# Performance work log

Measured on AMD Instinct MI355X. Metric: run time of the kernel, lower is better.

## Reference

```python
import jax, jax.numpy as jnp
import numpy as np

T, B, I, H = 128, 128, 256, 256  # numHiddenUnits(=seq len), batch, input_size, hidden_size


def setup_inputs() -> dict:
    key = jax.random.key(0)
    ks = jax.random.split(key, 7)
    stdv = 1.0 / np.sqrt(H)
    u = lambda k, shape: jax.random.uniform(k, shape, jnp.float32, -stdv, stdv)
    return {
        "batch_x": jax.random.normal(ks[0], (T, B, I), jnp.float32),
        "initial_state": jax.random.normal(ks[1], (B, H), jnp.float32),
        "initial_state_c": jax.random.normal(ks[2], (B, H), jnp.float32),
        # distinct weights per timestep (one LSTMCell per t), stacked on dim 0
        "W_input": u(ks[3], (T, I, 4 * H)),
        "B_input": u(ks[4], (T, 4 * H)),
        "W_hidden": u(ks[5], (T, H, 4 * H)),
        "B_hidden": u(ks[6], (T, 4 * H)),
    }


def reference(batch_x, initial_state, initial_state_c, W_input, B_input, W_hidden, B_hidden):
    def step(carry, xs):
        h, c = carry
        x_t, Wi, bi, Wh, bh = xs
        gates = x_t @ Wi + bi + h @ Wh + bh  # [B, 4H]
        i_t, f_t, o_t, g_t = jnp.split(gates, 4, axis=1)  # chunk order: i, f, o, c_tilde
        c = jax.nn.sigmoid(f_t) * c + jax.nn.sigmoid(i_t) * jnp.tanh(g_t)
        h = jax.nn.sigmoid(o_t) * jnp.tanh(c)
        return (h, c), h

    (h, c), outputs = jax.lax.scan(
        step, (initial_state, initial_state_c),
        (batch_x, W_input, B_input, W_hidden, B_hidden))
    return outputs, h, c  # outputs: [T, B, H]
```

## Files before the change

kernel.cpp:

```cpp
#include <hip/hip_runtime.h>
#include <hip/hip_bf16.h>
#include <cmath>

#define T_  128
#define B_  128
#define I_  256
#define H_  256
#define G4_ 1024

using frag  = __attribute__((ext_vector_type(8))) short;
using f32x4 = __attribute__((ext_vector_type(4))) float;

__device__ __forceinline__ unsigned short bf16u(float f) {
    __hip_bfloat16 b = __float2bfloat16(f);
    return __builtin_bit_cast(unsigned short, b);
}

#define BARRIER_SEQ() do {                                   \
    __builtin_amdgcn_sched_barrier(0);                       \
    asm volatile("s_waitcnt lgkmcnt(0)" ::: "memory");       \
    __builtin_amdgcn_s_barrier();                            \
    __builtin_amdgcn_sched_barrier(0);                       \
} while (0)

__global__ __launch_bounds__(256)
void lstm_pre(const float* __restrict__ x, const float* __restrict__ Wi,
              const float* __restrict__ bi, const float* __restrict__ bh,
              const float* __restrict__ Wh,
              float* __restrict__ Gxp, unsigned short* __restrict__ Whp)
{
    const int bid = blockIdx.x;
    const int tid = threadIdx.x;

    if (bid >= 4096) {
        int gid  = (bid - 4096) * 256 + tid;
        int lane = gid & 63;
        int nb   = (gid >> 6) & 63;
        int kb   = (gid >> 12) & 7;
        int t    = gid >> 15;
        int k0   = kb * 32 + (lane >> 4) * 8;
        int col  = nb * 16 + (lane & 15);
        const float* src = Wh + (size_t)(t * I_ + k0) * G4_ + col;
        unsigned short v[8];
        #pragma unroll
        for (int j = 0; j < 8; ++j) v[j] = bf16u(src[(size_t)j * G4_]);
        uint4 o;
        o.x = v[0] | ((unsigned)v[1] << 16);
        o.y = v[2] | ((unsigned)v[3] << 16);
        o.z = v[4] | ((unsigned)v[5] << 16);
        o.w = v[6] | ((unsigned)v[7] << 16);
        *(uint4*)(Whp + (size_t)gid * 8) = o;
        return;
    }

    __shared__ float xs[32][36];
    __shared__ float ws1[32][128];

    const int t  = bid >> 5;
    const int rt = (bid >> 3) & 3;
    const int cn = bid & 7;
    const int r0 = rt * 32;
    const int c0 = cn * 128;

    const int tr  = tid >> 5;
    const int tc4 = tid & 31;
    const int xrow = tid >> 3;
    const int xk0  = (tid & 7) * 4;

    float acc[4][4] = {};

    for (int kc = 0; kc < I_; kc += 32) {
        __syncthreads();
        *(float4*)&xs[xrow][xk0] =
            *(const float4*)&x[(t * B_ + r0 + xrow) * I_ + kc + xk0];
        #pragma unroll
        for (int q = 0; q < 4; ++q) {
            int s  = q * 256 + tid;
            int k  = s >> 5;
            int c4 = (s & 31) * 4;
            *(float4*)&ws1[k][c4] =
                *(const float4*)&Wi[(t * I_ + kc + k) * G4_ + c0 + c4];
        }
        __syncthreads();
        #pragma unroll
        for (int k = 0; k < 32; ++k) {
            float a0 = xs[tr * 4 + 0][k];
            float a1 = xs[tr * 4 + 1][k];
            float a2 = xs[tr * 4 + 2][k];
            float a3 = xs[tr * 4 + 3][k];
            float4 w4 = *(const float4*)&ws1[k][tc4 * 4];
            acc[0][0] += a0 * w4.x; acc[0][1] += a0 * w4.y; acc[0][2] += a0 * w4.z; acc[0][3] += a0 * w4.w;
            acc[1][0] += a1 * w4.x; acc[1][1] += a1 * w4.y; acc[1][2] += a1 * w4.z; acc[1][3] += a1 * w4.w;
            acc[2][0] += a2 * w4.x; acc[2][1] += a2 * w4.y; acc[2][2] += a2 * w4.z; acc[2][3] += a2 * w4.w;
            acc[3][0] += a3 * w4.x; acc[3][1] += a3 * w4.y; acc[3][2] += a3 * w4.z; acc[3][3] += a3 * w4.w;
        }
    }

    const int col = c0 + tc4 * 4;
    float4 b1 = *(const float4*)&bi[t * G4_ + col];
    float4 b2 = *(const float4*)&bh[t * G4_ + col];
    float bs[4] = {b1.x + b2.x, b1.y + b2.y, b1.z + b2.z, b1.w + b2.w};
    #pragma unroll
    for (int i = 0; i < 4; ++i) {
        const int gr   = r0 + tr * 4 + i;
        const int rb   = gr >> 4;
        const int rloc = gr & 15;
        #pragma unroll
        for (int j = 0; j < 4; ++j) {
            const int gc   = col + j;
            const int lane = (gc & 15) | ((rloc >> 2) << 4);
            Gxp[(((size_t)t * 8 + rb) * 64 + (gc >> 4)) * 256 + lane * 4 + (rloc & 3)]
                = acc[i][j] + bs[j];
        }
    }
}

__global__ __launch_bounds__(512, 1)
void lstm_rec(const float* __restrict__ h0, const float* __restrict__ c0in,
              const unsigned short* __restrict__ Whp,
              const float* __restrict__ Gxp, float* __restrict__ out,
              unsigned int* __restrict__ pub)
{
    __shared__ unsigned short h2[2][16][272];
    __shared__ float red[4][4][256];

    const int tid  = threadIdx.x;
    const int wv   = tid >> 6;
    const int lane = tid & 63;
    const int rg   = blockIdx.x & 7;
    const int sl   = blockIdx.x >> 3;
    const int r0   = rg * 16;
    const int oc0  = sl * 64;
    const int lrow = lane & 15;
    const int lhi  = lane >> 4;

    const int kh = wv >> 2;
    const int cb = wv & 3;

    {
        int row = tid >> 5;
        int cc  = (tid & 31) * 8;
        #pragma unroll
        for (int j = 0; j < 8; ++j)
            h2[0][row][cc + j] = bf16u(h0[(size_t)(r0 + row) * H_ + cc + j]);
    }

    float cst[4] = {0.f, 0.f, 0.f, 0.f};
    if (kh == 0) {
        #pragma unroll
        for (int rgi = 0; rgi < 4; ++rgi)
            cst[rgi] = c0in[(size_t)(r0 + lhi * 4 + rgi) * H_ + oc0 + cb * 16 + lrow];
    }

    int prow[12], pcol[12];
    if (kh == 1) {
        const int ltid = tid - 256;
        #pragma unroll
        for (int k = 0; k < 12; ++k) {
            int w  = ltid + k * 256;
            int rr = w / 192;
            int fc = w - rr * 192;
            prow[k] = rr;
            pcol[k] = fc + (fc >= oc0 ? 64 : 0);
        }
    }

    const unsigned short* wl = Whp + (size_t)lane * 8;
    const float*          gl = Gxp + (size_t)lane * 4;

    frag br[4][4];
    #pragma unroll
    for (int kbl = 0; kbl < 4; ++kbl)
        #pragma unroll
        for (int g = 0; g < 4; ++g)
            br[kbl][g] = *(const frag*)(wl +
                (size_t)((kh * 4 + kbl) * 64 + g * 16 + sl * 4 + cb) * 512);

    f32x4 gxr[4];
    if (kh == 0) {
        #pragma unroll
        for (int g = 0; g < 4; ++g)
            gxr[g] = *(const f32x4*)(gl +
                (size_t)((size_t)rg * 64 + g * 16 + sl * 4 + cb) * 256);
    }

    __syncthreads();

    for (int t = 0; t < T_; ++t) {
        f32x4 acc[4];
        if (kh == 0) {
            #pragma unroll
            for (int g = 0; g < 4; ++g) acc[g] = gxr[g];
            if (t + 1 < T_) {
                #pragma unroll
                for (int g = 0; g < 4; ++g)
                    gxr[g] = *(const f32x4*)(gl +
                        (size_t)(((t + 1) * 8 + rg) * 64 + g * 16 + sl * 4 + cb) * 256);
            }
        } else {
            #pragma unroll
            for (int g = 0; g < 4; ++g) acc[g] = (f32x4){0.f, 0.f, 0.f, 0.f};
        }

        #pragma unroll
        for (int kbl = 0; kbl < 4; ++kbl) {
            const int kb = kh * 4 + kbl;
            frag a = *(const frag*)&h2[t & 1][lrow][kb * 32 + lhi * 8];
            #pragma unroll
            for (int g = 0; g < 4; ++g)
                acc[g] = __builtin_amdgcn_mfma_f32_16x16x32_bf16(
                    a, br[kbl][g], acc[g], 0, 0, 0);
            if (t + 1 < T_) {
                #pragma unroll
                for (int g = 0; g < 4; ++g)
                    br[kbl][g] = *(const frag*)(wl +
                        (size_t)(((t + 1) * 8 + kb) * 64 + g * 16 + sl * 4 + cb) * 512);
            }
        }

        if (kh == 1) {
            #pragma unroll
            for (int g = 0; g < 4; ++g)
                *(f32x4*)&red[cb][g][lane * 4] = acc[g];
        }

        BARRIER_SEQ();

        if (kh == 0) {
            #pragma unroll
            for (int g = 0; g < 4; ++g)
                acc[g] += *(const f32x4*)&red[cb][g][lane * 4];
            const int colb = oc0 + cb * 16 + lrow;
            float hv[4];
            unsigned short hb[4];
            #pragma unroll
            for (int rgi = 0; rgi < 4; ++rgi) {
                float gi = acc[0][rgi], gf = acc[1][rgi];
                float go = acc[2][rgi], gg = acc[3][rgi];
                float i_ = __builtin_amdgcn_rcpf(1.f + __expf(-gi));
                float f_ = __builtin_amdgcn_rcpf(1.f + __expf(-gf));
                float o_ = __builtin_amdgcn_rcpf(1.f + __expf(-go));
                float gt = 1.f - 2.f * __builtin_amdgcn_rcpf(__expf(2.f * gg) + 1.f);
                float c  = f_ * cst[rgi] + i_ * gt;
                cst[rgi] = c;
                float tc = 1.f - 2.f * __builtin_amdgcn_rcpf(__expf(2.f * c) + 1.f);
                float h  = o_ * tc;
                hv[rgi] = h;
                hb[rgi] = bf16u(h);
            }
            if (t + 1 < T_) {
                #pragma unroll
                for (int rgi = 0; rgi < 4; ++rgi)
                    __hip_atomic_store(&pub[(size_t)(r0 + lhi * 4 + rgi) * H_ + colb],
                                       ((unsigned)(t + 1) << 16) | hb[rgi],
                                       __ATOMIC_RELAXED, __HIP_MEMORY_SCOPE_AGENT);
            }
            #pragma unroll
            for (int rgi = 0; rgi < 4; ++rgi) {
                const int row = lhi * 4 + rgi;
                out[(size_t)(t * B_ + r0 + row) * H_ + colb] = hv[rgi];
                h2[(t + 1) & 1][row][colb] = hb[rgi];
            }
            if (t == T_ - 1) {
                #pragma unroll
                for (int rgi = 0; rgi < 4; ++rgi) {
                    const int row = lhi * 4 + rgi;
                    out[(size_t)T_ * B_ * H_ + (size_t)(r0 + row) * H_ + colb] = hv[rgi];
                    out[(size_t)T_ * B_ * H_ + B_ * H_ + (size_t)(r0 + row) * H_ + colb] = cst[rgi];
                }
            }
        } else if (t + 1 < T_) {
            const unsigned want = (unsigned)(t + 1);
            while (true) {
                unsigned vv[12];
                #pragma unroll
                for (int k = 0; k < 12; ++k)
                    vv[k] = __hip_atomic_load(
                        &pub[(size_t)(r0 + prow[k]) * H_ + pcol[k]],
                        __ATOMIC_RELAXED, __HIP_MEMORY_SCOPE_AGENT);
                unsigned miss = 0;
                #pragma unroll
                for (int k = 0; k < 12; ++k) {
                    if ((vv[k] >> 16) == want)
                        h2[(t + 1) & 1][prow[k]][pcol[k]] =
                            (unsigned short)(vv[k] & 0xFFFFu);
                    else
                        miss = 1u;
                }
                if (!__any((int)miss)) break;
            }
        }

        BARRIER_SEQ();
    }
}

extern "C" void kernel_launch(void* const* d_in, const int* in_sizes, int n_in,
                              void* d_out, int out_size, void* d_ws, size_t ws_size,
                              hipStream_t stream) {
    const float* x  = (const float*)d_in[0];
    const float* h0 = (const float*)d_in[1];
    const float* c0 = (const float*)d_in[2];
    const float* Wi = (const float*)d_in[3];
    const float* bi = (const float*)d_in[4];
    const float* Wh = (const float*)d_in[5];
    const float* bh = (const float*)d_in[6];
    float* out = (float*)d_out;

    float*          Gxp = (float*)d_ws;
    unsigned short* Whp = (unsigned short*)((char*)d_ws + 67108864);
    unsigned int*   pub = (unsigned int*)((char*)d_ws + 134217728);

    hipMemsetAsync(pub, 0, 131072, stream);
    lstm_pre<<<dim3(4096 + 16384), dim3(256), 0, stream>>>(x, Wi, bi, bh, Wh, Gxp, Whp);
    lstm_rec<<<dim3(32), dim3(512), 0, stream>>>(h0, c0, Whp, Gxp, out, pub);
}
```

Measured before the change: 575.3 us.

## Fuse precompute and recurrence into one kernel with per-timestep readiness flags

Merges the input-projection GEMM, the Wh bf16 repacking kernel and the recurrent kernel into a single launch. The 32 recurrent blocks wait on per-timestep atomic counters published by producer blocks, so the recurrence can start while later timesteps are still being precomputed. The recurrent blocks also raise their wave priority. Producer blocks now use 512 threads handling two column tiles each. This aims to hide the preprocessing behind the serial recurrence, but it depends on the producer blocks for early timesteps being scheduled ahead of the others and on the recurrent blocks staying co-resident. Contention from producers may also slow the latency-bound recurrence.

New measurement: 849.2 us. 1.48x slower.

```diff
diff --git a/kernel.cpp b/kernel.cpp
--- a/kernel.cpp
+++ b/kernel.cpp
@@ -7,6 +7,10 @@
 #define I_  256
 #define H_  256
 #define G4_ 1024
+
+#define NREC   32
+#define P1_PER 16
+#define RP_PER 64
 
 using frag  = __attribute__((ext_vector_type(8))) short;
 using f32x4 = __attribute__((ext_vector_type(4))) float;
@@ -23,112 +27,131 @@
     __builtin_amdgcn_sched_barrier(0);                       \
 } while (0)
 
-__global__ __launch_bounds__(256)
-void lstm_pre(const float* __restrict__ x, const float* __restrict__ Wi,
+struct RecSmem {
+    unsigned short h2[2][16][272];
+    float red[4][4][256];
+};
+struct PreSmem {
+    float xs[32][36];
+    float ws1[2][32][128];
+};
+
+__global__ __launch_bounds__(512, 1)
+void lstm_all(const float* __restrict__ x, const float* __restrict__ Wi,
               const float* __restrict__ bi, const float* __restrict__ bh,
               const float* __restrict__ Wh,
-              float* __restrict__ Gxp, unsigned short* __restrict__ Whp)
+              const float* __restrict__ h0, const float* __restrict__ c0in,
+              float* __restrict__ Gxp, unsigned short* __restrict__ Whp,
+              float* __restrict__ out, unsigned int* __restrict__ pub,
+              int* __restrict__ dgx, int* __restrict__ dwh)
 {
+    __shared__ __align__(16) char smem_raw[sizeof(PreSmem)];
     const int bid = blockIdx.x;
     const int tid = threadIdx.x;
 
-    if (bid >= 4096) {
-        int gid  = (bid - 4096) * 256 + tid;
-        int lane = gid & 63;
-        int nb   = (gid >> 6) & 63;
-        int kb   = (gid >> 12) & 7;
-        int t    = gid >> 15;
-        int k0   = kb * 32 + (lane >> 4) * 8;
-        int col  = nb * 16 + (lane & 15);
-        const float* src = Wh + (size_t)(t * I_ + k0) * G4_ + col;
-        unsigned short v[8];
-        #pragma unroll
-        for (int j = 0; j < 8; ++j) v[j] = bf16u(src[(size_t)j * G4_]);
-        uint4 o;
-        o.x = v[0] | ((unsigned)v[1] << 16);
-        o.y = v[2] | ((unsigned)v[3] << 16);
-        o.z = v[4] | ((unsigned)v[5] << 16);
-        o.w = v[6] | ((unsigned)v[7] << 16);
-        *(uint4*)(Whp + (size_t)gid * 8) = o;
+    if (bid >= NREC) {
+        const int pbid = bid - NREC;
+        const int tt   = pbid / (P1_PER + RP_PER);
+        const int j    = pbid % (P1_PER + RP_PER);
+
+        if (j >= P1_PER) {
+            const int gid  = tt * 32768 + (j - P1_PER) * 512 + tid;
+            const int lane = gid & 63;
+            const int nb   = (gid >> 6) & 63;
+            const int kb   = (gid >> 12) & 7;
+            const int k0   = kb * 32 + (lane >> 4) * 8;
+            const int col  = nb * 16 + (lane & 15);
+            const float* src = Wh + (size_t)(tt * I_ + k0) * G4_ + col;
+            unsigned short v[8];
+            #pragma unroll
+            for (int jj = 0; jj < 8; ++jj) v[jj] = bf16u(src[(size_t)jj * G4_]);
+            uint4 o;
+            o.x = v[0] | ((unsigned)v[1] << 16);
+            o.y = v[2] | ((unsigned)v[3] << 16);
+            o.z = v[4] | ((unsigned)v[5] << 16);
+            o.w = v[6] | ((unsigned)v[7] << 16);
+            *(uint4*)(Whp + (size_t)gid * 8) = o;
+            __syncthreads();
+            if (tid == 0)
+                __hip_atomic_fetch_add(&dwh[tt], 1,
+                                       __ATOMIC_RELEASE, __HIP_MEMORY_SCOPE_AGENT);
+            return;
+        }
+
+        PreSmem* P = reinterpret_cast<PreSmem*>(smem_raw);
+        const int hb  = tid >> 8;
+        const int lt  = tid & 255;
+        const int rt  = j >> 2;
+        const int cn  = (j & 3) * 2 + hb;
+        const int r0  = rt * 32;
+        const int c0  = cn * 128;
+        const int tr  = lt >> 5;
+        const int tc4 = lt & 31;
+        const int xrow = lt >> 3;
+        const int xk0  = (lt & 7) * 4;
+
+        float acc[4][4] = {};
+
+        for (int kc = 0; kc < I_; kc += 32) {
+            __syncthreads();
+            if (hb == 0)
+                *(float4*)&P->xs[xrow][xk0] =
+                    *(const float4*)&x[(tt * B_ + r0 + xrow) * I_ + kc + xk0];
+            #pragma unroll
+            for (int q = 0; q < 4; ++q) {
+                int s  = q * 256 + lt;
+                int k  = s >> 5;
+                int c4 = (s & 31) * 4;
+                *(float4*)&P->ws1[hb][k][c4] =
+                    *(const float4*)&Wi[(size_t)(tt * I_ + kc + k) * G4_ + c0 + c4];
+            }
+            __syncthreads();
+            #pragma unroll
+            for (int k = 0; k < 32; ++k) {
+                float a0 = P->xs[tr * 4 + 0][k];
+                float a1 = P->xs[tr * 4 + 1][k];
+                float a2 = P->xs[tr * 4 + 2][k];
+                float a3 = P->xs[tr * 4 + 3][k];
+                float4 w4 = *(const float4*)&P->ws1[hb][k][tc4 * 4];
+                acc[0][0] += a0 * w4.x; acc[0][1] += a0 * w4.y; acc[0][2] += a0 * w4.z; acc[0][3] += a0 * w4.w;
+                acc[1][0] += a1 * w4.x; acc[1][1] += a1 * w4.y; acc[1][2] += a1 * w4.z; acc[1][3] += a1 * w4.w;
+                acc[2][0] += a2 * w4.x; acc[2][1] += a2 * w4.y; acc[2][2] += a2 * w4.z; acc[2][3] += a2 * w4.w;
+                acc[3][0] += a3 * w4.x; acc[3][1] += a3 * w4.y; acc[3][2] += a3 * w4.z; acc[3][3] += a3 * w4.w;
+            }
+        }
+
+        const int col = c0 + tc4 * 4;
+        float4 b1 = *(const float4*)&bi[(size_t)tt * G4_ + col];
+        float4 b2 = *(const float4*)&bh[(size_t)tt * G4_ + col];
+        float bs[4] = {b1.x + b2.x, b1.y + b2.y, b1.z + b2.z, b1.w + b2.w};
+        #pragma unroll
+        for (int i = 0; i < 4; ++i) {
+            const int gr   = r0 + tr * 4 + i;
+            const int rb   = gr >> 4;
+            const int rloc = gr & 15;
+            #pragma unroll
+            for (int jj = 0; jj < 4; ++jj) {
+                const int gc   = col + jj;
+                const int lane = (gc & 15) | ((rloc >> 2) << 4);
+                Gxp[(((size_t)tt * 8 + rb) * 64 + (gc >> 4)) * 256 + lane * 4 + (rloc & 3)]
+                    = acc[i][jj] + bs[jj];
+            }
+        }
+        __syncthreads();
+        if (tid == 0)
+            __hip_atomic_fetch_add(&dgx[tt], 1,
+                                   __ATOMIC_RELEASE, __HIP_MEMORY_SCOPE_AGENT);
         return;
     }
 
-    __shared__ float xs[32][36];
-    __shared__ float ws1[32][128];
-
-    const int t  = bid >> 5;
-    const int rt = (bid >> 3) & 3;
-    const int cn = bid & 7;
-    const int r0 = rt * 32;
-    const int c0 = cn * 128;
-
-    const int tr  = tid >> 5;
-    const int tc4 = tid & 31;
-    const int xrow = tid >> 3;
-    const int xk0  = (tid & 7) * 4;
-
-    float acc[4][4] = {};
-
-    for (int kc = 0; kc < I_; kc += 32) {
-        __syncthreads();
-        *(float4*)&xs[xrow][xk0] =
-            *(const float4*)&x[(t * B_ + r0 + xrow) * I_ + kc + xk0];
-        #pragma unroll
-        for (int q = 0; q < 4; ++q) {
-            int s  = q * 256 + tid;
-            int k  = s >> 5;
-            int c4 = (s & 31) * 4;
-            *(float4*)&ws1[k][c4] =
-                *(const float4*)&Wi[(t * I_ + kc + k) * G4_ + c0 + c4];
-        }
-        __syncthreads();
-        #pragma unroll
-        for (int k = 0; k < 32; ++k) {
-            float a0 = xs[tr * 4 + 0][k];
-            float a1 = xs[tr * 4 + 1][k];
-            float a2 = xs[tr * 4 + 2][k];
-            float a3 = xs[tr * 4 + 3][k];
-            float4 w4 = *(const float4*)&ws1[k][tc4 * 4];
-            acc[0][0] += a0 * w4.x; acc[0][1] += a0 * w4.y; acc[0][2] += a0 * w4.z; acc[0][3] += a0 * w4.w;
-            acc[1][0] += a1 * w4.x; acc[1][1] += a1 * w4.y; acc[1][2] += a1 * w4.z; acc[1][3] += a1 * w4.w;
-            acc[2][0] += a2 * w4.x; acc[2][1] += a2 * w4.y; acc[2][2] += a2 * w4.z; acc[2][3] += a2 * w4.w;
-            acc[3][0] += a3 * w4.x; acc[3][1] += a3 * w4.y; acc[3][2] += a3 * w4.z; acc[3][3] += a3 * w4.w;
-        }
-    }
-
-    const int col = c0 + tc4 * 4;
-    float4 b1 = *(const float4*)&bi[t * G4_ + col];
-    float4 b2 = *(const float4*)&bh[t * G4_ + col];
-    float bs[4] = {b1.x + b2.x, b1.y + b2.y, b1.z + b2.z, b1.w + b2.w};
-    #pragma unroll
-    for (int i = 0; i < 4; ++i) {
-        const int gr   = r0 + tr * 4 + i;
-        const int rb   = gr >> 4;
-        const int rloc = gr & 15;
-        #pragma unroll
-        for (int j = 0; j < 4; ++j) {
-            const int gc   = col + j;
-            const int lane = (gc & 15) | ((rloc >> 2) << 4);
-            Gxp[(((size_t)t * 8 + rb) * 64 + (gc >> 4)) * 256 + lane * 4 + (rloc & 3)]
-                = acc[i][j] + bs[j];
-        }
-    }
-}
-
-__global__ __launch_bounds__(512, 1)
-void lstm_rec(const float* __restrict__ h0, const float* __restrict__ c0in,
-              const unsigned short* __restrict__ Whp,
-              const float* __restrict__ Gxp, float* __restrict__ out,
-              unsigned int* __restrict__ pub)
-{
-    __shared__ unsigned short h2[2][16][272];
-    __shared__ float red[4][4][256];
-
-    const int tid  = threadIdx.x;
+    __builtin_amdgcn_s_setprio(1);
+
+    RecSmem* R = reinterpret_cast<RecSmem*>(smem_raw);
+
     const int wv   = tid >> 6;
     const int lane = tid & 63;
-    const int rg   = blockIdx.x & 7;
-    const int sl   = blockIdx.x >> 3;
+    const int rg   = bid & 7;
+    const int sl   = bid >> 3;
     const int r0   = rg * 16;
     const int oc0  = sl * 64;
     const int lrow = lane & 15;
@@ -141,8 +164,8 @@
         int row = tid >> 5;
         int cc  = (tid & 31) * 8;
         #pragma unroll
-        for (int j = 0; j < 8; ++j)
-            h2[0][row][cc + j] = bf16u(h0[(size_t)(r0 + row) * H_ + cc + j]);
+        for (int jj = 0; jj < 8; ++jj)
+            R->h2[0][row][cc + jj] = bf16u(h0[(size_t)(r0 + row) * H_ + cc + jj]);
     }
 
     float cst[4] = {0.f, 0.f, 0.f, 0.f};
@@ -168,6 +191,19 @@
     const unsigned short* wl = Whp + (size_t)lane * 8;
     const float*          gl = Gxp + (size_t)lane * 4;
 
+    __syncthreads();
+
+    if (wv == 0) {
+        for (int tn = 0; tn < 2; ++tn) {
+            while (true) {
+                int a = __hip_atomic_load(&dgx[tn], __ATOMIC_ACQUIRE, __HIP_MEMORY_SCOPE_AGENT);
+                int b = __hip_atomic_load(&dwh[tn], __ATOMIC_ACQUIRE, __HIP_MEMORY_SCOPE_AGENT);
+                if (a >= P1_PER && b >= RP_PER) break;
+            }
+        }
+    }
+    __syncthreads();
+
     frag br[4][4];
     #pragma unroll
     for (int kbl = 0; kbl < 4; ++kbl)
@@ -184,8 +220,6 @@
                 (size_t)((size_t)rg * 64 + g * 16 + sl * 4 + cb) * 256);
     }
 
-    __syncthreads();
-
     for (int t = 0; t < T_; ++t) {
         f32x4 acc[4];
         if (kh == 0) {
@@ -205,7 +239,7 @@
         #pragma unroll
         for (int kbl = 0; kbl < 4; ++kbl) {
             const int kb = kh * 4 + kbl;
-            frag a = *(const frag*)&h2[t & 1][lrow][kb * 32 + lhi * 8];
+            frag a = *(const frag*)&R->h2[t & 1][lrow][kb * 32 + lhi * 8];
             #pragma unroll
             for (int g = 0; g < 4; ++g)
                 acc[g] = __builtin_amdgcn_mfma_f32_16x16x32_bf16(
@@ -221,7 +255,7 @@
         if (kh == 1) {
             #pragma unroll
             for (int g = 0; g < 4; ++g)
-                *(f32x4*)&red[cb][g][lane * 4] = acc[g];
+                *(f32x4*)&R->red[cb][g][lane * 4] = acc[g];
         }
 
         BARRIER_SEQ();
@@ -229,7 +263,7 @@
         if (kh == 0) {
             #pragma unroll
             for (int g = 0; g < 4; ++g)
-                acc[g] += *(const f32x4*)&red[cb][g][lane * 4];
+                acc[g] += *(const f32x4*)&R->red[cb][g][lane * 4];
             const int colb = oc0 + cb * 16 + lrow;
             float hv[4];
             unsigned short hb[4];
@@ -259,7 +293,7 @@
             for (int rgi = 0; rgi < 4; ++rgi) {
                 const int row = lhi * 4 + rgi;
                 out[(size_t)(t * B_ + r0 + row) * H_ + colb] = hv[rgi];
-                h2[(t + 1) & 1][row][colb] = hb[rgi];
+                R->h2[(t + 1) & 1][row][colb] = hb[rgi];
             }
             if (t == T_ - 1) {
                 #pragma unroll
@@ -269,6 +303,13 @@
                     out[(size_t)T_ * B_ * H_ + B_ * H_ + (size_t)(r0 + row) * H_ + colb] = cst[rgi];
                 }
             }
+            if (wv == 0 && t + 2 < T_) {
+                while (true) {
+                    int a = __hip_atomic_load(&dgx[t + 2], __ATOMIC_ACQUIRE, __HIP_MEMORY_SCOPE_AGENT);
+                    int b = __hip_atomic_load(&dwh[t + 2], __ATOMIC_ACQUIRE, __HIP_MEMORY_SCOPE_AGENT);
+                    if (a >= P1_PER && b >= RP_PER) break;
+                }
+            }
         } else if (t + 1 < T_) {
             const unsigned want = (unsigned)(t + 1);
             while (true) {
@@ -282,7 +323,7 @@
                 #pragma unroll
                 for (int k = 0; k < 12; ++k) {
                     if ((vv[k] >> 16) == want)
-                        h2[(t + 1) & 1][prow[k]][pcol[k]] =
+                        R->h2[(t + 1) & 1][prow[k]][pcol[k]] =
                             (unsigned short)(vv[k] & 0xFFFFu);
                     else
                         miss = 1u;
@@ -310,8 +351,11 @@
     float*          Gxp = (float*)d_ws;
     unsigned short* Whp = (unsigned short*)((char*)d_ws + 67108864);
     unsigned int*   pub = (unsigned int*)((char*)d_ws + 134217728);
-
-    hipMemsetAsync(pub, 0, 131072, stream);
-    lstm_pre<<<dim3(4096 + 16384), dim3(256), 0, stream>>>(x, Wi, bi, bh, Wh, Gxp, Whp);
-    lstm_rec<<<dim3(32), dim3(512), 0, stream>>>(h0, c0, Whp, Gxp, out, pub);
+    int*            dgx = (int*)((char*)d_ws + 134217728 + 131072);
+    int*            dwh = (int*)((char*)d_ws + 134217728 + 131072 + 512);
+
+    hipMemsetAsync(pub, 0, 131072 + 1024, stream);
+    const int nprod = T_ * (P1_PER + RP_PER);
+    lstm_all<<<dim3(NREC + nprod), dim3(512), 0, stream>>>(
+        x, Wi, bi, bh, Wh, h0, c0, Gxp, Whp, out, pub, dgx, dwh);
 }
```
